# Optimization experiments

Measured on AMD Instinct MI355X. Metric: run time of the kernel, lower is better.

## Reference

```python
import jax, jax.numpy as jnp
import numpy as np
import math

B, T, C, H = 4, 1024, 1024, 16
D = C // H
EPS = 1e-5


def layer_norm(x, w, b):
    mu = jnp.mean(x, axis=-1, keepdims=True)
    var = jnp.mean(jnp.square(x - mu), axis=-1, keepdims=True)
    return (x - mu) * jax.lax.rsqrt(var + EPS) * w + b


def setup_inputs() -> dict:
    key = jax.random.key(0)
    ks = jax.random.split(key, 8)
    s = 0.02
    return {
        "x": jax.random.normal(ks[0], (B, T, C), jnp.float32),
        "attention_mask": jnp.ones((B, T), jnp.float32),
        "ln1_w": jnp.ones((C,), jnp.float32),
        "ln1_b": jnp.zeros((C,), jnp.float32),
        "w_attn": jax.random.normal(ks[1], (C, 3 * C), jnp.float32) * s,
        "b_attn": jnp.zeros((3 * C,), jnp.float32),
        "w_proj": jax.random.normal(ks[2], (C, C), jnp.float32) * s,
        "b_proj": jnp.zeros((C,), jnp.float32),
        "threshold": jnp.float32(0.0005),  # (layer_idx+1)/n_layer * final_token_threshold
        "ln2_w": jnp.ones((C,), jnp.float32),
        "ln2_b": jnp.zeros((C,), jnp.float32),
        "w_fc": jax.random.normal(ks[3], (C, 4 * C), jnp.float32) * s,
        "b_fc": jnp.zeros((4 * C,), jnp.float32),
        "w_fc2": jax.random.normal(ks[4], (4 * C, C), jnp.float32) * s,
        "b_fc2": jnp.zeros((C,), jnp.float32),
    }


def reference(x, attention_mask, ln1_w, ln1_b, w_attn, b_attn, w_proj, b_proj,
              threshold, ln2_w, ln2_b, w_fc, b_fc, w_fc2, b_fc2):
    # ---- attention (eval mode, dropout=0; hard masking_mode) ----
    h = layer_norm(x, ln1_w, ln1_b)
    qkv = h @ w_attn + b_attn                      # (B,T,3C)
    q, k, v = jnp.split(qkv, 3, axis=-1)
    q = q.reshape(B, T, H, D).transpose(0, 2, 1, 3)  # (B,H,T,D)
    k = k.reshape(B, T, H, D).transpose(0, 2, 1, 3)
    v = v.reshape(B, T, H, D).transpose(0, 2, 1, 3)

    scale = 1.0 / math.sqrt(D)
    logits = jnp.einsum("bhqd,bhkd->bhqk", q, k) * scale  # (B,H,T,T)
    causal = jnp.tril(jnp.ones((T, T), bool))
    neg_inf = jnp.float32(-jnp.inf)
    logits = jnp.where(causal[None, None], logits, neg_inf)
    # key-side validity mask (applied in original's manual pass; mask is all-ones
    # here so flash-path y == softmax(causal logits) @ v as well)
    logits = jnp.where(attention_mask[:, None, None, :] == 0, neg_inf, logits)
    att = jax.nn.softmax(logits, axis=-1)

    y = jnp.einsum("bhqk,bhkd->bhqd", att, v)      # (B,H,T,D)
    importance = att.mean(axis=1).mean(axis=1)     # (B,T): mean over heads, then queries

    y = y.transpose(0, 2, 1, 3).reshape(B, T, C)
    x = x + (y @ w_proj + b_proj)

    # ---- hard pruning mask ----
    pruning_mask = (importance >= threshold).astype(x.dtype)
    combined_mask = attention_mask * pruning_mask
    x = x * combined_mask[:, :, None]

    # ---- MLP ----
    h2 = layer_norm(x, ln2_w, ln2_b)
    f = jax.nn.gelu(h2 @ w_fc + b_fc, approximate=False)
    x = x + (f @ w_fc2 + b_fc2)

    pruning_loss = jnp.float32(0.0)  # hard mode -> always 0
    return (x, combined_mask, pruning_loss)
```

## Files before the change

### kernel.cpp

```cpp
#include <hip/hip_runtime.h>
#include <cstdint>
#include <cstring>

typedef unsigned short u16;
typedef short bf16x8 __attribute__((ext_vector_type(8)));
typedef float f32x4 __attribute__((ext_vector_type(4)));

#define MFMA16(a,b,c) __builtin_amdgcn_mfma_f32_16x16x32_bf16(a,b,c,0,0,0)


__device__ __forceinline__ u16 f2bf(float f) {
  union { float f; uint32_t u; } un; un.f = f;
  uint32_t u = un.u;
  u += 0x7FFFu + ((u >> 16) & 1u);
  return (u16)(u >> 16);
}

__device__ __forceinline__ float bf2f(u16 h) {
  union { uint32_t u; float f; } un; un.u = ((uint32_t)h) << 16;
  return un.f;
}

__device__ __forceinline__ float gelu_fast(float v) {
  float u = 0.7978845608028654f * (v + 0.044715f * v * v * v);
  float e = __expf(2.f * u);
  float th = 1.f - __fdividef(2.f, e + 1.f);
  return 0.5f * v * (1.f + th);
}

__device__ __forceinline__ void gl_lds16(const void* g, void* l) {
  __builtin_amdgcn_global_load_lds(
      (__attribute__((address_space(1))) void*)(const_cast<void*>(g)),
      (__attribute__((address_space(3))) void*)l, 16, 0, 0);
}


__global__ __launch_bounds__(256) void transpose_all(
    const float* __restrict__ wa, const float* __restrict__ wp,
    const float* __restrict__ wf, const float* __restrict__ wf2,
    u16* __restrict__ wat, u16* __restrict__ wpt,
    u16* __restrict__ wft, u16* __restrict__ wf2t)
{
  __shared__ float tile[32][33];
  int id = blockIdx.x;
  const float* W; u16* Wt; int K, N, bx, by;
  if (id < 3072)      { W = wa;  Wt = wat;  K = 1024; N = 3072; bx = id % 96;  by = id / 96; }
  else if (id < 4096) { id -= 3072; W = wp;  Wt = wpt;  K = 1024; N = 1024; bx = id % 32; by = id / 32; }
  else if (id < 8192) { id -= 4096; W = wf;  Wt = wft;  K = 1024; N = 4096; bx = id % 128; by = id / 128; }
  else                { id -= 8192; W = wf2; Wt = wf2t; K = 4096; N = 1024; bx = id % 32; by = id / 32; }
  int kt = by * 32, nt = bx * 32;
  int tx = threadIdx.x, ty = threadIdx.y;
#pragma unroll
  for (int i = 0; i < 4; ++i)
    tile[ty + i * 8][tx] = W[(size_t)(kt + ty + i * 8) * N + nt + tx];
  __syncthreads();
#pragma unroll
  for (int i = 0; i < 4; ++i)
    Wt[(size_t)(nt + ty + i * 8) * K + kt + tx] = f2bf(tile[tx][ty + i * 8]);
}


__global__ __launch_bounds__(256) void ln_bf16(
    const float* __restrict__ x, const float* __restrict__ wt,
    const float* __restrict__ bs, u16* __restrict__ out)
{
  int row = blockIdx.x;
  int tid = threadIdx.x, lane = tid & 63, w = tid >> 6;
  const float* xr = x + (size_t)row * 1024;
  float4 v = *(const float4*)(xr + tid * 4);
  float s = v.x + v.y + v.z + v.w;
  float sq = v.x * v.x + v.y * v.y + v.z * v.z + v.w * v.w;
#pragma unroll
  for (int o = 1; o < 64; o <<= 1) { s += __shfl_xor(s, o); sq += __shfl_xor(sq, o); }
  __shared__ float ls[4], lq[4];
  if (lane == 0) { ls[w] = s; lq[w] = sq; }
  __syncthreads();
  s = ls[0] + ls[1] + ls[2] + ls[3];
  sq = lq[0] + lq[1] + lq[2] + lq[3];
  float mu = s * (1.f / 1024.f);
  float var = sq * (1.f / 1024.f) - mu * mu;
  float rstd = rsqrtf(var + 1e-5f);
  float4 wv = *(const float4*)(wt + tid * 4);
  float4 bv = *(const float4*)(bs + tid * 4);
  ushort4 o4;
  o4.x = f2bf((v.x - mu) * rstd * wv.x + bv.x);
  o4.y = f2bf((v.y - mu) * rstd * wv.y + bv.y);
  o4.z = f2bf((v.z - mu) * rstd * wv.z + bv.z);
  o4.w = f2bf((v.w - mu) * rstd * wv.w + bv.w);
  *(ushort4*)(out + (size_t)row * 1024 + tid * 4) = o4;
}


__device__ __forceinline__ void gemm256_mainloop(
    const char* __restrict__ Ab, const char* __restrict__ Bb,
    size_t sA, size_t sB, int nT,
    f32x4 acc[8][4], u16* lA, u16* lB)
{
  const int tid = threadIdx.x;
  const int lane = tid & 63, w = tid >> 6;
  const int laneM = lane & 15, q4 = lane >> 4;
  const int wr = w >> 2, wc = w & 3;

#pragma unroll
  for (int i = 0; i < 8; ++i)
#pragma unroll
    for (int j = 0; j < 4; ++j)
      acc[i][j] = f32x4{0.f, 0.f, 0.f, 0.f};

  const int ch = (((tid & 3) ^ ((tid >> 3) & 3)) << 4);
  const char* srcA0 = Ab + (size_t)(tid >> 2) * sA + ch;
  const char* srcA1 = srcA0 + (size_t)128 * sA;
  const char* srcB0 = Bb + (size_t)(tid >> 2) * sB + ch;
  const char* srcB1 = srcB0 + (size_t)128 * sB;
  char* dA0 = (char*)lA + tid * 16;
  char* dB0 = (char*)lB + tid * 16;

  const int swz = ((q4 ^ ((laneM >> 1) & 3)) << 4);
  const char* rdA = (const char*)lA + (wr * 128 + laneM) * 64 + swz;
  const char* rdB = (const char*)lB + (wc * 64 + laneM) * 64 + swz;

#pragma unroll
  for (int t = 0; t < 3; ++t) {
    gl_lds16(srcA0 + t * 64, dA0 + t * 16384);
    gl_lds16(srcA1 + t * 64, dA0 + t * 16384 + 8192);
    gl_lds16(srcB0 + t * 64, dB0 + t * 16384);
    gl_lds16(srcB1 + t * 64, dB0 + t * 16384 + 8192);
  }
  asm volatile("s_waitcnt vmcnt(8)" ::: "memory");
  __builtin_amdgcn_s_barrier();
  asm volatile("" ::: "memory");

  for (int t = 0; t < nT; ++t) {
    const int cb = (t & 3) << 14;
    const int sb = ((t + 3) & 3) << 14;
    const bool st = (t + 3) < nT;
    const char* rA = rdA + cb;
    const char* rB = rdB + cb;

    bf16x8 aF[4], bF[4];
#pragma unroll
    for (int i = 0; i < 4; ++i) aF[i] = *(const bf16x8*)(rA + i * 1024);
#pragma unroll
    for (int i = 0; i < 4; ++i) bF[i] = *(const bf16x8*)(rB + i * 1024);
    if (st) {
      gl_lds16(srcA0 + (size_t)(t + 3) * 64, dA0 + sb);
      gl_lds16(srcA1 + (size_t)(t + 3) * 64, dA0 + sb + 8192);
    }
    __builtin_amdgcn_s_barrier();
    asm volatile("s_waitcnt lgkmcnt(0)" ::: "memory");
    __builtin_amdgcn_s_setprio(1);
#pragma unroll
    for (int i = 0; i < 4; ++i)
#pragma unroll
      for (int j = 0; j < 4; ++j)
        acc[i][j] = MFMA16(aF[i], bF[j], acc[i][j]);
    __builtin_amdgcn_s_setprio(0);
    __builtin_amdgcn_s_barrier();
    asm volatile("" ::: "memory");

    bf16x8 aG[4];
#pragma unroll
    for (int i = 0; i < 4; ++i) aG[i] = *(const bf16x8*)(rA + 4096 + i * 1024);
    if (st) {
      gl_lds16(srcB0 + (size_t)(t + 3) * 64, dB0 + sb);
      gl_lds16(srcB1 + (size_t)(t + 3) * 64, dB0 + sb + 8192);
    }
    __builtin_amdgcn_s_barrier();
    asm volatile("s_waitcnt lgkmcnt(0)" ::: "memory");
    __builtin_amdgcn_s_setprio(1);
#pragma unroll
    for (int i = 0; i < 4; ++i)
#pragma unroll
      for (int j = 0; j < 4; ++j)
        acc[4 + i][j] = MFMA16(aG[i], bF[j], acc[4 + i][j]);
    __builtin_amdgcn_s_setprio(0);
    if (t + 4 <= nT)      asm volatile("s_waitcnt vmcnt(8)" ::: "memory");
    else if (t + 3 == nT) asm volatile("s_waitcnt vmcnt(4)" ::: "memory");
    else                  asm volatile("s_waitcnt vmcnt(0)" ::: "memory");
    __builtin_amdgcn_s_barrier();
    asm volatile("" ::: "memory");
  }
}


__device__ __forceinline__ void gemm_mainloop_db(
    const u16* __restrict__ Abase, const u16* __restrict__ Bbase,
    int lda, int ldb, int nIter, f32x4 acc[4][4])
{
  __shared__ __align__(16) u16 lA[2][128 * 32];
  __shared__ __align__(16) u16 lB[2][128 * 32];

  const int tid = threadIdx.x;
  const int lane = tid & 63;
  const int w = tid >> 6;
  const int wr = (w >> 1) * 64;
  const int wc = (w & 1) * 64;
  const int laneM = lane & 15;
  const int laneK = (lane >> 4) * 8;

#pragma unroll
  for (int i = 0; i < 4; ++i)
#pragma unroll
    for (int j = 0; j < 4; ++j)
      acc[i][j] = f32x4{0.f, 0.f, 0.f, 0.f};

  const int off0 = w * 1024 + lane * 16;
  const int off1 = off0 + 4096;
  const int rA0 = off0 >> 6, cb0 = off0 & 63;
  const int rA1 = off1 >> 6, cb1 = off1 & 63;

  const size_t sA = (size_t)lda * 2;
  const size_t sB = (size_t)ldb * 2;
  const char* pA0 = (const char*)Abase + (size_t)rA0 * sA + cb0;
  const char* pA1 = (const char*)Abase + (size_t)rA1 * sA + cb1;
  const char* pB0 = (const char*)Bbase + (size_t)rA0 * sB + cb0;
  const char* pB1 = (const char*)Bbase + (size_t)rA1 * sB + cb1;
  char* dA0 = (char*)&lA[0][0] + off0;
  char* dA1 = (char*)&lA[0][0] + off1;
  char* dB0 = (char*)&lB[0][0] + off0;
  char* dB1 = (char*)&lB[0][0] + off1;

  gl_lds16(pA0, dA0); gl_lds16(pA1, dA1);
  gl_lds16(pB0, dB0); gl_lds16(pB1, dB1);
  pA0 += 64; pA1 += 64; pB0 += 64; pB1 += 64;
  __syncthreads();

  for (int it = 0; it < nIter; ++it) {
    const int cur = it & 1;
    const int nb = cur ^ 1;
    if (it + 1 < nIter) {
      gl_lds16(pA0, dA0 + nb * 8192);
      gl_lds16(pA1, dA1 + nb * 8192);
      gl_lds16(pB0, dB0 + nb * 8192);
      gl_lds16(pB1, dB1 + nb * 8192);
      pA0 += 64; pA1 += 64; pB0 += 64; pB1 += 64;
    }
    const u16* aRd = &lA[cur][(wr + laneM) * 32 + laneK];
    const u16* bRd = &lB[cur][(wc + laneM) * 32 + laneK];
    bf16x8 af[4], bfr[4];
#pragma unroll
    for (int t = 0; t < 4; ++t) {
      af[t]  = *(const bf16x8*)(aRd + t * 16 * 32);
      bfr[t] = *(const bf16x8*)(bRd + t * 16 * 32);
    }
#pragma unroll
    for (int i = 0; i < 4; ++i)
#pragma unroll
      for (int j = 0; j < 4; ++j)
        acc[i][j] = MFMA16(af[i], bfr[j], acc[i][j]);
    if (it + 1 < nIter) __syncthreads();
  }
}


__global__ __launch_bounds__(512, 2) void gemm_qkv(
    const u16* __restrict__ A, const u16* __restrict__ Bt,
    const float* __restrict__ bias,
    u16* __restrict__ qo, u16* __restrict__ ko, u16* __restrict__ vo)
{
  __shared__ __align__(16) u16 lA[4][8192];
  __shared__ __align__(16) u16 lB[4][8192];
  const int id = blockIdx.x;
  const int my = ((id & 7) << 1) | ((id >> 3) & 1);
  const int nx = id >> 4;
  const int m0 = my * 256, n0 = nx * 256;
  f32x4 acc[8][4];
  gemm256_mainloop((const char*)(A + (size_t)m0 * 1024),
                   (const char*)(Bt + (size_t)n0 * 1024),
                   2048, 2048, 32, acc, &lA[0][0], &lB[0][0]);

  const int lane = threadIdx.x & 63, w = threadIdx.x >> 6;
  const int wr = w >> 2, wc = w & 3;
  const int laneM = lane & 15, q4 = lane >> 4;
  const int which = n0 >> 10;
#pragma unroll
  for (int fr = 0; fr < 8; ++fr) {
#pragma unroll
    for (int fc = 0; fc < 4; ++fc) {
      int n = n0 + wc * 64 + fc * 16 + laneM;
      int c = n & 1023;
      int hh = c >> 6, d = c & 63;
      float bval = bias[n];
      if (which == 2) {
        int m0r = m0 + wr * 128 + fr * 16 + q4 * 4;
        int b = m0r >> 10, t0 = m0r & 1023;
        ushort4 o4;
        o4.x = f2bf(acc[fr][fc][0] + bval);
        o4.y = f2bf(acc[fr][fc][1] + bval);
        o4.z = f2bf(acc[fr][fc][2] + bval);
        o4.w = f2bf(acc[fr][fc][3] + bval);
        *(ushort4*)&vo[((size_t)((b * 16 + hh) * 64 + d)) * 1024 + t0] = o4;
      } else {
        u16* dst = (which == 0) ? qo : ko;
#pragma unroll
        for (int r = 0; r < 4; ++r) {
          int m = m0 + wr * 128 + fr * 16 + q4 * 4 + r;
          int b = m >> 10, t = m & 1023;
          dst[((size_t)((b * 16 + hh) * 1024 + t)) * 64 + d] = f2bf(acc[fr][fc][r] + bval);
        }
      }
    }
  }
}

__global__ __launch_bounds__(256, 4) void gemm_proj(
    const u16* __restrict__ A, const u16* __restrict__ Bt,
    const float* __restrict__ bias, const float* __restrict__ xin,
    const float* __restrict__ maskv, float* __restrict__ x2)
{
  f32x4 acc[4][4];
  int m0 = blockIdx.y * 128, n0 = blockIdx.x * 128;
  gemm_mainloop_db(A + (size_t)m0 * 1024, Bt + (size_t)n0 * 1024, 1024, 1024, 32, acc);
  const int lane = threadIdx.x & 63, w = threadIdx.x >> 6;
  const int wr = (w >> 1) * 64, wc = (w & 1) * 64;
  const int laneM = lane & 15, q4 = lane >> 4;
#pragma unroll
  for (int ti = 0; ti < 4; ++ti) {
#pragma unroll
    for (int tj = 0; tj < 4; ++tj) {
      int n = n0 + wc + tj * 16 + laneM;
      float bval = bias[n];
#pragma unroll
      for (int r = 0; r < 4; ++r) {
        int m = m0 + wr + ti * 16 + q4 * 4 + r;
        float v = xin[(size_t)m * 1024 + n] + acc[ti][tj][r] + bval;
        x2[(size_t)m * 1024 + n] = v * maskv[m];
      }
    }
  }
}

__global__ __launch_bounds__(512, 2) void gemm_fc(
    const u16* __restrict__ A, const u16* __restrict__ Bt,
    const float* __restrict__ bias, u16* __restrict__ fo)
{
  __shared__ __align__(16) u16 lA[4][8192];
  __shared__ __align__(16) u16 lB[4][8192];
  const int id = blockIdx.x;
  const int my = ((id & 7) << 1) | ((id >> 3) & 1);
  const int nx = id >> 4;
  const int m0 = my * 256, n0 = nx * 256;
  f32x4 acc[8][4];
  gemm256_mainloop((const char*)(A + (size_t)m0 * 1024),
                   (const char*)(Bt + (size_t)n0 * 1024),
                   2048, 2048, 32, acc, &lA[0][0], &lB[0][0]);

  const int lane = threadIdx.x & 63, w = threadIdx.x >> 6;
  const int wr = w >> 2, wc = w & 3;
  const int laneM = lane & 15, q4 = lane >> 4;
#pragma unroll
  for (int fr = 0; fr < 8; ++fr) {
#pragma unroll
    for (int fc = 0; fc < 4; ++fc) {
      int n = n0 + wc * 64 + fc * 16 + laneM;
      float bval = bias[n];
#pragma unroll
      for (int r = 0; r < 4; ++r) {
        int m = m0 + wr * 128 + fr * 16 + q4 * 4 + r;
        fo[(size_t)m * 4096 + n] = f2bf(gelu_fast(acc[fr][fc][r] + bval));
      }
    }
  }
}

__global__ __launch_bounds__(512, 2) void gemm_fc2_splitk(
    const u16* __restrict__ A, const u16* __restrict__ Bt,
    u16* __restrict__ pall)
{
  __shared__ __align__(16) u16 lA[4][8192];
  __shared__ __align__(16) u16 lB[4][8192];
  const int id = blockIdx.x;
  const int cmb = (id & 7) | (((id >> 7) & 1) << 3);
  const int mt = (id >> 3) & 15;
  const int n0 = (cmb & 3) * 256;
  const int kz = cmb >> 2;
  const int m0 = mt * 256;
  f32x4 acc[8][4];
  gemm256_mainloop((const char*)(A + (size_t)m0 * 4096 + kz * 1024),
                   (const char*)(Bt + (size_t)n0 * 4096 + kz * 1024),
                   8192, 8192, 32, acc, &lA[0][0], &lB[0][0]);

  u16* p = pall + (size_t)kz * 4096 * 1024;
  const int lane = threadIdx.x & 63, w = threadIdx.x >> 6;
  const int wr = w >> 2, wc = w & 3;
  const int laneM = lane & 15, q4 = lane >> 4;
#pragma unroll
  for (int fr = 0; fr < 8; ++fr) {
#pragma unroll
    for (int fc = 0; fc < 4; ++fc) {
      int n = n0 + wc * 64 + fc * 16 + laneM;
#pragma unroll
      for (int r = 0; r < 4; ++r) {
        int m = m0 + wr * 128 + fr * 16 + q4 * 4 + r;
        p[(size_t)m * 1024 + n] = f2bf(acc[fr][fc][r]);
      }
    }
  }
}

__global__ __launch_bounds__(256) void fc2_finalize(
    const float* __restrict__ x2, const float* __restrict__ bias,
    const u16* __restrict__ pall, float* __restrict__ out)
{
  int i = blockIdx.x * 256 + threadIdx.x;
  int col4 = i & 255;
  float4 a = ((const float4*)x2)[i];
  float4 b = ((const float4*)bias)[col4];
  float s0 = a.x + b.x, s1 = a.y + b.y, s2 = a.z + b.z, s3 = a.w + b.w;
#pragma unroll
  for (int z = 0; z < 4; ++z) {
    ushort4 u = ((const ushort4*)(pall + (size_t)z * 4194304))[i];
    s0 += bf2f(u.x); s1 += bf2f(u.y); s2 += bf2f(u.z); s3 += bf2f(u.w);
  }
  float4 o; o.x = s0; o.y = s1; o.z = s2; o.w = s3;
  ((float4*)out)[i] = o;
}


__global__ __launch_bounds__(512) void attn_fwd(
    const u16* __restrict__ qb, const u16* __restrict__ kb, const u16* __restrict__ vtb,
    u16* __restrict__ yb, float* __restrict__ part)
{
  const int id = blockIdx.x;
  const int slot = (id & 7) ^ ((id >> 8) & 1);
  const int qbi = (slot & 1) ? (slot >> 1) : (7 - (slot >> 1));
  const int bh = id >> 3;
  const int b = bh >> 4, h = bh & 15;

  const int tid = threadIdx.x, lane = tid & 63, w = tid >> 6;
  const int q0 = qbi * 128;
  const int laneM = lane & 15, q4 = lane >> 4;
  const float scale = 0.125f;

  __shared__ __align__(16) u16 lK[2][64 * 72];
  __shared__ __align__(16) u16 lV[2][64 * 72];
  __shared__ __align__(16) u16 lP[8][16 * 72];
  __shared__ float part_s[1024];

  part_s[tid] = 0.f;
  part_s[tid + 512] = 0.f;

  bf16x8 qf[2];
  {
    const u16* qrow = qb + ((size_t)(bh * 1024 + q0 + w * 16 + laneM)) * 64 + q4 * 8;
    qf[0] = *(const bf16x8*)qrow;
    qf[1] = *(const bf16x8*)(qrow + 32);
  }

  const int nkt = 2 * qbi + 2;
  const int srow = tid >> 3;
  const int scol = (tid & 7) * 8;
  const u16* kbase = kb + (size_t)bh * 65536;
  const u16* vbase = vtb + (size_t)bh * 65536;

  float lrow[4] = {0.f, 0.f, 0.f, 0.f};
  {
    uint4 pk = *(const uint4*)(kbase + (size_t)srow * 64 + scol);
    *(uint4*)&lK[0][srow * 72 + scol] = pk;
    __syncthreads();
    for (int kt = 0; kt < nkt; ++kt) {
      const int cur = kt & 1;
      if (kt + 1 < nkt)
        pk = *(const uint4*)(kbase + (size_t)((kt + 1) * 64 + srow) * 64 + scol);
#pragma unroll
      for (int tj = 0; tj < 4; ++tj) {
        const u16* kp = &lK[cur][(tj * 16 + laneM) * 72 + q4 * 8];
        bf16x8 k0 = *(const bf16x8*)kp;
        bf16x8 k1 = *(const bf16x8*)(kp + 32);
        f32x4 z = {0.f, 0.f, 0.f, 0.f};
        z = MFMA16(qf[0], k0, z);
        z = MFMA16(qf[1], k1, z);
        int kc = kt * 64 + tj * 16 + laneM;
#pragma unroll
        for (int r = 0; r < 4; ++r) {
          int qg = q0 + w * 16 + q4 * 4 + r;
          lrow[r] += (kc <= qg) ? __expf(z[r] * scale) : 0.f;
        }
      }
      if (kt + 1 < nkt) *(uint4*)&lK[cur ^ 1][srow * 72 + scol] = pk;
      __syncthreads();
    }
  }
  float linv[4];
#pragma unroll
  for (int r = 0; r < 4; ++r) {
    float s = lrow[r];
    s += __shfl_xor(s, 1); s += __shfl_xor(s, 2);
    s += __shfl_xor(s, 4); s += __shfl_xor(s, 8);
    linv[r] = 1.f / s;
  }

  f32x4 o_[4];
#pragma unroll
  for (int dt = 0; dt < 4; ++dt) o_[dt] = f32x4{0.f, 0.f, 0.f, 0.f};

  {
    uint4 pk = *(const uint4*)(kbase + (size_t)srow * 64 + scol);
    uint4 pv = *(const uint4*)(vbase + (size_t)srow * 1024 + scol);
    *(uint4*)&lK[0][srow * 72 + scol] = pk;
    *(uint4*)&lV[0][srow * 72 + scol] = pv;
    __syncthreads();
    for (int kt = 0; kt < nkt; ++kt) {
      const int cur = kt & 1;
      if (kt + 1 < nkt) {
        pk = *(const uint4*)(kbase + (size_t)((kt + 1) * 64 + srow) * 64 + scol);
        pv = *(const uint4*)(vbase + (size_t)srow * 1024 + (kt + 1) * 64 + scol);
      }
      u16* lPw = &lP[w][0];
#pragma unroll
      for (int tj = 0; tj < 4; ++tj) {
        const u16* kp = &lK[cur][(tj * 16 + laneM) * 72 + q4 * 8];
        bf16x8 k0 = *(const bf16x8*)kp;
        bf16x8 k1 = *(const bf16x8*)(kp + 32);
        f32x4 z = {0.f, 0.f, 0.f, 0.f};
        z = MFMA16(qf[0], k0, z);
        z = MFMA16(qf[1], k1, z);
        int kc = kt * 64 + tj * 16 + laneM;
        float cs = 0.f;
#pragma unroll
        for (int r = 0; r < 4; ++r) {
          int qg = q0 + w * 16 + q4 * 4 + r;
          float pvf = (kc <= qg) ? __expf(z[r] * scale) * linv[r] : 0.f;
          cs += pvf;
          lPw[(q4 * 4 + r) * 72 + tj * 16 + laneM] = f2bf(pvf);
        }
        cs += __shfl_xor(cs, 16);
        cs += __shfl_xor(cs, 32);
        if (lane < 16) atomicAdd(&part_s[kt * 64 + tj * 16 + lane], cs);
      }
#pragma unroll
      for (int ss = 0; ss < 2; ++ss) {
        bf16x8 pf = *(const bf16x8*)&lP[w][laneM * 72 + ss * 32 + q4 * 8];
#pragma unroll
        for (int dt = 0; dt < 4; ++dt) {
          bf16x8 vf = *(const bf16x8*)&lV[cur][(dt * 16 + laneM) * 72 + ss * 32 + q4 * 8];
          o_[dt] = MFMA16(pf, vf, o_[dt]);
        }
      }
      if (kt + 1 < nkt) {
        *(uint4*)&lK[cur ^ 1][srow * 72 + scol] = pk;
        *(uint4*)&lV[cur ^ 1][srow * 72 + scol] = pv;
      }
      __syncthreads();
    }
  }

  const int kmax = nkt * 64;
  for (int i = tid; i < kmax; i += 512)
    atomicAdd(&part[(size_t)bh * 1024 + i], part_s[i]);

#pragma unroll
  for (int dt = 0; dt < 4; ++dt)
#pragma unroll
    for (int r = 0; r < 4; ++r) {
      int qg = q0 + w * 16 + q4 * 4 + r;
      yb[((size_t)(b * 1024 + qg)) * 1024 + h * 64 + dt * 16 + laneM] = f2bf(o_[dt][r]);
    }
}


__global__ __launch_bounds__(256) void finalize_mask(
    const float* __restrict__ part, const float* __restrict__ amask,
    const float* __restrict__ thr, float* __restrict__ mask_ws,
    float* __restrict__ out_mask, float* __restrict__ out_loss)
{
  int i = blockIdx.x * 256 + threadIdx.x;
  if (i >= 4096) return;
  int b = i >> 10;
  int t = i & 1023;
  float s = 0.f;
#pragma unroll
  for (int hh = 0; hh < 16; ++hh) s += part[(size_t)(b * 16 + hh) * 1024 + t];
  float imp = s * (1.0f / 16384.0f);
  float mv = (imp >= thr[0]) ? amask[i] : 0.f;
  mask_ws[i] = mv;
  out_mask[i] = mv;
  if (i == 0) out_loss[0] = 0.f;
}


extern "C" void kernel_launch(void* const* d_in, const int* in_sizes, int n_in,
                              void* d_out, int out_size, void* d_ws, size_t ws_size,
                              hipStream_t stream) {
  const float* x      = (const float*)d_in[0];
  const float* amask  = (const float*)d_in[1];
  const float* ln1w   = (const float*)d_in[2];
  const float* ln1b   = (const float*)d_in[3];
  const float* w_attn = (const float*)d_in[4];
  const float* b_attn = (const float*)d_in[5];
  const float* w_proj = (const float*)d_in[6];
  const float* b_proj = (const float*)d_in[7];
  const float* thr    = (const float*)d_in[8];
  const float* ln2w   = (const float*)d_in[9];
  const float* ln2b   = (const float*)d_in[10];
  const float* w_fc   = (const float*)d_in[11];
  const float* b_fc   = (const float*)d_in[12];
  const float* w_fc2  = (const float*)d_in[13];
  const float* b_fc2  = (const float*)d_in[14];
  float* out = (float*)d_out;

  char* ws = (char*)d_ws;
  size_t off = 0;
  auto alloc = [&](size_t bytes) -> char* {
    char* p = ws + off;
    off += (bytes + 255) & ~(size_t)255;
    return p;
  };
  u16* wattnT = (u16*)alloc((size_t)3072 * 1024 * 2);
  u16* wprojT = (u16*)alloc((size_t)1024 * 1024 * 2);
  u16* wfcT   = (u16*)alloc((size_t)4096 * 1024 * 2);
  u16* wfc2T  = (u16*)alloc((size_t)1024 * 4096 * 2);
  u16* hbuf   = (u16*)alloc((size_t)4096 * 1024 * 2);
  u16* qbuf   = (u16*)alloc((size_t)64 * 1024 * 64 * 2);
  u16* kbuf   = (u16*)alloc((size_t)64 * 1024 * 64 * 2);
  u16* vtbuf  = (u16*)alloc((size_t)64 * 64 * 1024 * 2);
  u16* ybuf   = (u16*)alloc((size_t)4096 * 1024 * 2);
  float* part = (float*)alloc((size_t)64 * 1024 * 4);
  float* maskws = (float*)alloc((size_t)4096 * 4);
  float* x2   = (float*)alloc((size_t)4096 * 1024 * 4);
  u16* h2     = (u16*)alloc((size_t)4096 * 1024 * 2);
  u16* fbuf   = (u16*)alloc((size_t)4096 * 4096 * 2);

  u16* pall = qbuf;

  transpose_all<<<12288, dim3(32, 8), 0, stream>>>(
      w_attn, w_proj, w_fc, w_fc2, wattnT, wprojT, wfcT, wfc2T);

  hipMemsetAsync(part, 0, (size_t)64 * 1024 * 4, stream);

  ln_bf16<<<4096, 256, 0, stream>>>(x, ln1w, ln1b, hbuf);

  gemm_qkv<<<192, 512, 0, stream>>>(hbuf, wattnT, b_attn, qbuf, kbuf, vtbuf);

  attn_fwd<<<512, 512, 0, stream>>>(qbuf, kbuf, vtbuf, ybuf, part);

  finalize_mask<<<16, 256, 0, stream>>>(part, amask, thr, maskws,
                                        out + 4194304, out + 4198400);

  gemm_proj<<<dim3(8, 32), 256, 0, stream>>>(ybuf, wprojT, b_proj, x, maskws, x2);

  ln_bf16<<<4096, 256, 0, stream>>>(x2, ln2w, ln2b, h2);

  gemm_fc<<<256, 512, 0, stream>>>(h2, wfcT, b_fc, fbuf);

  gemm_fc2_splitk<<<256, 512, 0, stream>>>(fbuf, wfc2T, pall);

  fc2_finalize<<<4096, 256, 0, stream>>>(x2, b_fc2, pall, out);
}
```

Measured before the change: 354.5 us.

## Retile FC GEMM to 128x128, swizzle LDS loads, widen transpose, add priorities

After: 352.2 us. Within noise of the previous version (-0.6%).

```diff
diff --git a/kernel.cpp b/kernel.cpp
--- a/kernel.cpp
+++ b/kernel.cpp
@@ -7,6 +7,7 @@
 typedef float f32x4 __attribute__((ext_vector_type(4)));
 
 #define MFMA16(a,b,c) __builtin_amdgcn_mfma_f32_16x16x32_bf16(a,b,c,0,0,0)
+#define SBAR0() __builtin_amdgcn_sched_barrier(0)
 
 
 __device__ __forceinline__ u16 f2bf(float f) {
@@ -41,22 +42,36 @@
     u16* __restrict__ wat, u16* __restrict__ wpt,
     u16* __restrict__ wft, u16* __restrict__ wf2t)
 {
-  __shared__ float tile[32][33];
+  __shared__ float tile[64][65];
   int id = blockIdx.x;
   const float* W; u16* Wt; int K, N, bx, by;
-  if (id < 3072)      { W = wa;  Wt = wat;  K = 1024; N = 3072; bx = id % 96;  by = id / 96; }
-  else if (id < 4096) { id -= 3072; W = wp;  Wt = wpt;  K = 1024; N = 1024; bx = id % 32; by = id / 32; }
-  else if (id < 8192) { id -= 4096; W = wf;  Wt = wft;  K = 1024; N = 4096; bx = id % 128; by = id / 128; }
-  else                { id -= 8192; W = wf2; Wt = wf2t; K = 4096; N = 1024; bx = id % 32; by = id / 32; }
-  int kt = by * 32, nt = bx * 32;
-  int tx = threadIdx.x, ty = threadIdx.y;
-#pragma unroll
-  for (int i = 0; i < 4; ++i)
-    tile[ty + i * 8][tx] = W[(size_t)(kt + ty + i * 8) * N + nt + tx];
+  if (id < 768)       { W = wa;  Wt = wat;  K = 1024; N = 3072; bx = id % 48; by = id / 48; }
+  else if (id < 1024) { id -= 768;  W = wp;  Wt = wpt;  K = 1024; N = 1024; bx = id % 16; by = id / 16; }
+  else if (id < 2048) { id -= 1024; W = wf;  Wt = wft;  K = 1024; N = 4096; bx = id % 64; by = id / 64; }
+  else                { id -= 2048; W = wf2; Wt = wf2t; K = 4096; N = 1024; bx = id % 16; by = id / 16; }
+  int kt = by * 64, nt = bx * 64;
+  int tid = threadIdx.x;
+  int tx = tid & 15, ty = tid >> 4;
+#pragma unroll
+  for (int i = 0; i < 4; ++i) {
+    int r = ty + i * 16;
+    float4 v = *(const float4*)&W[(size_t)(kt + r) * N + nt + tx * 4];
+    tile[r][tx * 4 + 0] = v.x;
+    tile[r][tx * 4 + 1] = v.y;
+    tile[r][tx * 4 + 2] = v.z;
+    tile[r][tx * 4 + 3] = v.w;
+  }
   __syncthreads();
 #pragma unroll
-  for (int i = 0; i < 4; ++i)
-    Wt[(size_t)(nt + ty + i * 8) * K + kt + tx] = f2bf(tile[tx][ty + i * 8]);
+  for (int i = 0; i < 4; ++i) {
+    int n = ty + i * 16;
+    ushort4 o4;
+    o4.x = f2bf(tile[tx * 4 + 0][n]);
+    o4.y = f2bf(tile[tx * 4 + 1][n]);
+    o4.z = f2bf(tile[tx * 4 + 2][n]);
+    o4.w = f2bf(tile[tx * 4 + 3][n]);
+    *(ushort4*)&Wt[(size_t)(nt + n) * K + kt + tx * 4] = o4;
+  }
 }
 
 
@@ -91,98 +106,6 @@
 }
 
 
-__device__ __forceinline__ void gemm256_mainloop(
-    const char* __restrict__ Ab, const char* __restrict__ Bb,
-    size_t sA, size_t sB, int nT,
-    f32x4 acc[8][4], u16* lA, u16* lB)
-{
-  const int tid = threadIdx.x;
-  const int lane = tid & 63, w = tid >> 6;
-  const int laneM = lane & 15, q4 = lane >> 4;
-  const int wr = w >> 2, wc = w & 3;
-
-#pragma unroll
-  for (int i = 0; i < 8; ++i)
-#pragma unroll
-    for (int j = 0; j < 4; ++j)
-      acc[i][j] = f32x4{0.f, 0.f, 0.f, 0.f};
-
-  const int ch = (((tid & 3) ^ ((tid >> 3) & 3)) << 4);
-  const char* srcA0 = Ab + (size_t)(tid >> 2) * sA + ch;
-  const char* srcA1 = srcA0 + (size_t)128 * sA;
-  const char* srcB0 = Bb + (size_t)(tid >> 2) * sB + ch;
-  const char* srcB1 = srcB0 + (size_t)128 * sB;
-  char* dA0 = (char*)lA + tid * 16;
-  char* dB0 = (char*)lB + tid * 16;
-
-  const int swz = ((q4 ^ ((laneM >> 1) & 3)) << 4);
-  const char* rdA = (const char*)lA + (wr * 128 + laneM) * 64 + swz;
-  const char* rdB = (const char*)lB + (wc * 64 + laneM) * 64 + swz;
-
-#pragma unroll
-  for (int t = 0; t < 3; ++t) {
-    gl_lds16(srcA0 + t * 64, dA0 + t * 16384);
-    gl_lds16(srcA1 + t * 64, dA0 + t * 16384 + 8192);
-    gl_lds16(srcB0 + t * 64, dB0 + t * 16384);
-    gl_lds16(srcB1 + t * 64, dB0 + t * 16384 + 8192);
-  }
-  asm volatile("s_waitcnt vmcnt(8)" ::: "memory");
-  __builtin_amdgcn_s_barrier();
-  asm volatile("" ::: "memory");
-
-  for (int t = 0; t < nT; ++t) {
-    const int cb = (t & 3) << 14;
-    const int sb = ((t + 3) & 3) << 14;
-    const bool st = (t + 3) < nT;
-    const char* rA = rdA + cb;
-    const char* rB = rdB + cb;
-
-    bf16x8 aF[4], bF[4];
-#pragma unroll
-    for (int i = 0; i < 4; ++i) aF[i] = *(const bf16x8*)(rA + i * 1024);
-#pragma unroll
-    for (int i = 0; i < 4; ++i) bF[i] = *(const bf16x8*)(rB + i * 1024);
-    if (st) {
-      gl_lds16(srcA0 + (size_t)(t + 3) * 64, dA0 + sb);
-      gl_lds16(srcA1 + (size_t)(t + 3) * 64, dA0 + sb + 8192);
-    }
-    __builtin_amdgcn_s_barrier();
-    asm volatile("s_waitcnt lgkmcnt(0)" ::: "memory");
-    __builtin_amdgcn_s_setprio(1);
-#pragma unroll
-    for (int i = 0; i < 4; ++i)
-#pragma unroll
-      for (int j = 0; j < 4; ++j)
-        acc[i][j] = MFMA16(aF[i], bF[j], acc[i][j]);
-    __builtin_amdgcn_s_setprio(0);
-    __builtin_amdgcn_s_barrier();
-    asm volatile("" ::: "memory");
-
-    bf16x8 aG[4];
-#pragma unroll
-    for (int i = 0; i < 4; ++i) aG[i] = *(const bf16x8*)(rA + 4096 + i * 1024);
-    if (st) {
-      gl_lds16(srcB0 + (size_t)(t + 3) * 64, dB0 + sb);
-      gl_lds16(srcB1 + (size_t)(t + 3) * 64, dB0 + sb + 8192);
-    }
-    __builtin_amdgcn_s_barrier();
-    asm volatile("s_waitcnt lgkmcnt(0)" ::: "memory");
-    __builtin_amdgcn_s_setprio(1);
-#pragma unroll
-    for (int i = 0; i < 4; ++i)
-#pragma unroll
-      for (int j = 0; j < 4; ++j)
-        acc[4 + i][j] = MFMA16(aG[i], bF[j], acc[4 + i][j]);
-    __builtin_amdgcn_s_setprio(0);
-    if (t + 4 <= nT)      asm volatile("s_waitcnt vmcnt(8)" ::: "memory");
-    else if (t + 3 == nT) asm volatile("s_waitcnt vmcnt(4)" ::: "memory");
-    else                  asm volatile("s_waitcnt vmcnt(0)" ::: "memory");
-    __builtin_amdgcn_s_barrier();
-    asm volatile("" ::: "memory");
-  }
-}
-
-
 __device__ __forceinline__ void gemm_mainloop_db(
     const u16* __restrict__ Abase, const u16* __restrict__ Bbase,
     int lda, int ldb, int nIter, f32x4 acc[4][4])
@@ -196,7 +119,7 @@
   const int wr = (w >> 1) * 64;
   const int wc = (w & 1) * 64;
   const int laneM = lane & 15;
-  const int laneK = (lane >> 4) * 8;
+  const int q4 = lane >> 4;
 
 #pragma unroll
   for (int i = 0; i < 4; ++i)
@@ -206,15 +129,16 @@
 
   const int off0 = w * 1024 + lane * 16;
   const int off1 = off0 + 4096;
-  const int rA0 = off0 >> 6, cb0 = off0 & 63;
-  const int rA1 = off1 >> 6, cb1 = off1 & 63;
+  const int rA0 = off0 >> 6;
+  const int rA1 = off1 >> 6;
+  const int scb = (((lane & 3) ^ ((lane >> 3) & 3)) << 4);
 
   const size_t sA = (size_t)lda * 2;
   const size_t sB = (size_t)ldb * 2;
-  const char* pA0 = (const char*)Abase + (size_t)rA0 * sA + cb0;
-  const char* pA1 = (const char*)Abase + (size_t)rA1 * sA + cb1;
-  const char* pB0 = (const char*)Bbase + (size_t)rA0 * sB + cb0;
-  const char* pB1 = (const char*)Bbase + (size_t)rA1 * sB + cb1;
+  const char* pA0 = (const char*)Abase + (size_t)rA0 * sA + scb;
+  const char* pA1 = (const char*)Abase + (size_t)rA1 * sA + scb;
+  const char* pB0 = (const char*)Bbase + (size_t)rA0 * sB + scb;
+  const char* pB1 = (const char*)Bbase + (size_t)rA1 * sB + scb;
   char* dA0 = (char*)&lA[0][0] + off0;
   char* dA1 = (char*)&lA[0][0] + off1;
   char* dB0 = (char*)&lB[0][0] + off0;
@@ -224,6 +148,8 @@
   gl_lds16(pB0, dB0); gl_lds16(pB1, dB1);
   pA0 += 64; pA1 += 64; pB0 += 64; pB1 += 64;
   __syncthreads();
+
+  const int rdswz = ((q4 ^ ((laneM >> 1) & 3)) << 4);
 
   for (int it = 0; it < nIter; ++it) {
     const int cur = it & 1;
@@ -235,13 +161,13 @@
       gl_lds16(pB1, dB1 + nb * 8192);
       pA0 += 64; pA1 += 64; pB0 += 64; pB1 += 64;
     }
-    const u16* aRd = &lA[cur][(wr + laneM) * 32 + laneK];
-    const u16* bRd = &lB[cur][(wc + laneM) * 32 + laneK];
+    const char* aRd = (const char*)&lA[cur][0] + (wr + laneM) * 64 + rdswz;
+    const char* bRd = (const char*)&lB[cur][0] + (wc + laneM) * 64 + rdswz;
     bf16x8 af[4], bfr[4];
 #pragma unroll
     for (int t = 0; t < 4; ++t) {
-      af[t]  = *(const bf16x8*)(aRd + t * 16 * 32);
-      bfr[t] = *(const bf16x8*)(bRd + t * 16 * 32);
+      af[t]  = *(const bf16x8*)(aRd + t * 1024);
+      bfr[t] = *(const bf16x8*)(bRd + t * 1024);
     }
 #pragma unroll
     for (int i = 0; i < 4; ++i)
@@ -249,6 +175,106 @@
       for (int j = 0; j < 4; ++j)
         acc[i][j] = MFMA16(af[i], bfr[j], acc[i][j]);
     if (it + 1 < nIter) __syncthreads();
+  }
+}
+
+
+__device__ __forceinline__ void gemm256_mainloop(
+    const char* __restrict__ Ab, const char* __restrict__ Bb,
+    size_t sA, size_t sB, int nT,
+    f32x4 acc[8][4], u16* lA, u16* lB)
+{
+  const int tid = threadIdx.x;
+  const int lane = tid & 63, w = tid >> 6;
+  const int laneM = lane & 15, q4 = lane >> 4;
+  const int wr = w >> 2, wc = w & 3;
+
+#pragma unroll
+  for (int i = 0; i < 8; ++i)
+#pragma unroll
+    for (int j = 0; j < 4; ++j)
+      acc[i][j] = f32x4{0.f, 0.f, 0.f, 0.f};
+
+  const int ch = (((tid & 3) ^ ((tid >> 3) & 3)) << 4);
+  const char* srcA0 = Ab + (size_t)(tid >> 2) * sA + ch;
+  const char* srcA1 = srcA0 + (size_t)128 * sA;
+  const char* srcB0 = Bb + (size_t)(tid >> 2) * sB + ch;
+  const char* srcB1 = srcB0 + (size_t)128 * sB;
+  char* dA0 = (char*)lA + tid * 16;
+  char* dB0 = (char*)lB + tid * 16;
+
+  const int swz = ((q4 ^ ((laneM >> 1) & 3)) << 4);
+  const char* rdA = (const char*)lA + (wr * 128 + laneM) * 64 + swz;
+  const char* rdB = (const char*)lB + (wc * 64 + laneM) * 64 + swz;
+
+#pragma unroll
+  for (int t = 0; t < 3; ++t) {
+    gl_lds16(srcA0 + t * 64, dA0 + t * 16384);
+    gl_lds16(srcA1 + t * 64, dA0 + t * 16384 + 8192);
+    gl_lds16(srcB0 + t * 64, dB0 + t * 16384);
+    gl_lds16(srcB1 + t * 64, dB0 + t * 16384 + 8192);
+  }
+  asm volatile("s_waitcnt vmcnt(8)" ::: "memory");
+  SBAR0();
+  __builtin_amdgcn_s_barrier();
+  SBAR0();
+
+  for (int t = 0; t < nT; ++t) {
+    const int cb = (t & 3) << 14;
+    const int sb = ((t + 3) & 3) << 14;
+    const bool st = (t + 3) < nT;
+    const char* rA = rdA + cb;
+    const char* rB = rdB + cb;
+
+    bf16x8 aF[4], bF[4];
+#pragma unroll
+    for (int i = 0; i < 4; ++i) aF[i] = *(const bf16x8*)(rA + i * 1024);
+#pragma unroll
+    for (int i = 0; i < 4; ++i) bF[i] = *(const bf16x8*)(rB + i * 1024);
+    if (st) {
+      gl_lds16(srcA0 + (size_t)(t + 3) * 64, dA0 + sb);
+      gl_lds16(srcA1 + (size_t)(t + 3) * 64, dA0 + sb + 8192);
+    }
+    SBAR0();
+    __builtin_amdgcn_s_barrier();
+    asm volatile("s_waitcnt lgkmcnt(0)" ::: "memory");
+    SBAR0();
+    __builtin_amdgcn_s_setprio(1);
+#pragma unroll
+    for (int i = 0; i < 4; ++i)
+#pragma unroll
+      for (int j = 0; j < 4; ++j)
+        acc[i][j] = MFMA16(aF[i], bF[j], acc[i][j]);
+    __builtin_amdgcn_s_setprio(0);
+    SBAR0();
+    __builtin_amdgcn_s_barrier();
+    SBAR0();
+
+    bf16x8 aG[4];
+#pragma unroll
+    for (int i = 0; i < 4; ++i) aG[i] = *(const bf16x8*)(rA + 4096 + i * 1024);
+    if (st) {
+      gl_lds16(srcB0 + (size_t)(t + 3) * 64, dB0 + sb);
+      gl_lds16(srcB1 + (size_t)(t + 3) * 64, dB0 + sb + 8192);
+    }
+    SBAR0();
+    __builtin_amdgcn_s_barrier();
+    asm volatile("s_waitcnt lgkmcnt(0)" ::: "memory");
+    SBAR0();
+    __builtin_amdgcn_s_setprio(1);
+#pragma unroll
+    for (int i = 0; i < 4; ++i)
+#pragma unroll
+      for (int j = 0; j < 4; ++j)
+        acc[4 + i][j] = MFMA16(aG[i], bF[j], acc[4 + i][j]);
+    __builtin_amdgcn_s_setprio(0);
+    SBAR0();
+    if (t + 4 <= nT)      asm volatile("s_waitcnt vmcnt(8)" ::: "memory");
+    else if (t + 3 == nT) asm volatile("s_waitcnt vmcnt(4)" ::: "memory");
+    else                  asm volatile("s_waitcnt vmcnt(0)" ::: "memory");
+    SBAR0();
+    __builtin_amdgcn_s_barrier();
+    SBAR0();
   }
 }
 
@@ -330,34 +356,26 @@
   }
 }
 
-__global__ __launch_bounds__(512, 2) void gemm_fc(
+__global__ __launch_bounds__(256, 4) void gemm_fc(
     const u16* __restrict__ A, const u16* __restrict__ Bt,
     const float* __restrict__ bias, u16* __restrict__ fo)
 {
-  __shared__ __align__(16) u16 lA[4][8192];
-  __shared__ __align__(16) u16 lB[4][8192];
-  const int id = blockIdx.x;
-  const int my = ((id & 7) << 1) | ((id >> 3) & 1);
-  const int nx = id >> 4;
-  const int m0 = my * 256, n0 = nx * 256;
-  f32x4 acc[8][4];
-  gemm256_mainloop((const char*)(A + (size_t)m0 * 1024),
-                   (const char*)(Bt + (size_t)n0 * 1024),
-                   2048, 2048, 32, acc, &lA[0][0], &lB[0][0]);
-
+  f32x4 acc[4][4];
+  int m0 = blockIdx.y * 128, n0 = blockIdx.x * 128;
+  gemm_mainloop_db(A + (size_t)m0 * 1024, Bt + (size_t)n0 * 1024, 1024, 1024, 32, acc);
   const int lane = threadIdx.x & 63, w = threadIdx.x >> 6;
-  const int wr = w >> 2, wc = w & 3;
+  const int wr = (w >> 1) * 64, wc = (w & 1) * 64;
   const int laneM = lane & 15, q4 = lane >> 4;
 #pragma unroll
-  for (int fr = 0; fr < 8; ++fr) {
-#pragma unroll
-    for (int fc = 0; fc < 4; ++fc) {
-      int n = n0 + wc * 64 + fc * 16 + laneM;
+  for (int ti = 0; ti < 4; ++ti) {
+#pragma unroll
+    for (int tj = 0; tj < 4; ++tj) {
+      int n = n0 + wc + tj * 16 + laneM;
       float bval = bias[n];
 #pragma unroll
       for (int r = 0; r < 4; ++r) {
-        int m = m0 + wr * 128 + fr * 16 + q4 * 4 + r;
-        fo[(size_t)m * 4096 + n] = f2bf(gelu_fast(acc[fr][fc][r] + bval));
+        int m = m0 + wr + ti * 16 + q4 * 4 + r;
+        fo[(size_t)m * 4096 + n] = f2bf(gelu_fast(acc[ti][tj][r] + bval));
       }
     }
   }
@@ -468,8 +486,10 @@
         bf16x8 k0 = *(const bf16x8*)kp;
         bf16x8 k1 = *(const bf16x8*)(kp + 32);
         f32x4 z = {0.f, 0.f, 0.f, 0.f};
+        __builtin_amdgcn_s_setprio(1);
         z = MFMA16(qf[0], k0, z);
         z = MFMA16(qf[1], k1, z);
+        __builtin_amdgcn_s_setprio(0);
         int kc = kt * 64 + tj * 16 + laneM;
 #pragma unroll
         for (int r = 0; r < 4; ++r) {
@@ -513,8 +533,10 @@
         bf16x8 k0 = *(const bf16x8*)kp;
         bf16x8 k1 = *(const bf16x8*)(kp + 32);
         f32x4 z = {0.f, 0.f, 0.f, 0.f};
+        __builtin_amdgcn_s_setprio(1);
         z = MFMA16(qf[0], k0, z);
         z = MFMA16(qf[1], k1, z);
+        __builtin_amdgcn_s_setprio(0);
         int kc = kt * 64 + tj * 16 + laneM;
         float cs = 0.f;
 #pragma unroll
@@ -528,6 +550,7 @@
         cs += __shfl_xor(cs, 32);
         if (lane < 16) atomicAdd(&part_s[kt * 64 + tj * 16 + lane], cs);
       }
+      __builtin_amdgcn_s_setprio(1);
 #pragma unroll
       for (int ss = 0; ss < 2; ++ss) {
         bf16x8 pf = *(const bf16x8*)&lP[w][laneM * 72 + ss * 32 + q4 * 8];
@@ -537,6 +560,7 @@
           o_[dt] = MFMA16(pf, vf, o_[dt]);
         }
       }
+      __builtin_amdgcn_s_setprio(0);
       if (kt + 1 < nkt) {
         *(uint4*)&lK[cur ^ 1][srow * 72 + scol] = pk;
         *(uint4*)&lV[cur ^ 1][srow * 72 + scol] = pv;
@@ -623,7 +647,7 @@
 
   u16* pall = qbuf;
 
-  transpose_all<<<12288, dim3(32, 8), 0, stream>>>(
+  transpose_all<<<3072, 256, 0, stream>>>(
       w_attn, w_proj, w_fc, w_fc2, wattnT, wprojT, wfcT, wfc2T);
 
   hipMemsetAsync(part, 0, (size_t)64 * 1024 * 4, stream);
@@ -641,7 +665,7 @@
 
   ln_bf16<<<4096, 256, 0, stream>>>(x2, ln2w, ln2b, h2);
 
-  gemm_fc<<<256, 512, 0, stream>>>(h2, wfcT, b_fc, fbuf);
+  gemm_fc<<<dim3(32, 32), 256, 0, stream>>>(h2, wfcT, b_fc, fbuf);
 
   gemm_fc2_splitk<<<256, 512, 0, stream>>>(fbuf, wfc2T, pall);
 
```
